# Kernel tuning notes

Hardware: AMD Instinct MI355X
Metric: run time of the kernel (lower is better)

## Reference

```python
import jax, jax.numpy as jnp
import numpy as np

NEG = -1e30  # effective -inf that stays finite in fp32 under cumsum


def _log_semiring_scan(m, v):
    """Solve a[u] = logaddexp(v[u], m[u] + a[u-1]) along the last axis
    via an associative scan in the (logaddexp, +) semiring."""
    def op(a, b):
        am, av = a
        bm, bv = b
        return (am + bm, jnp.logaddexp(bv, bm + av))
    return jax.lax.associative_scan(op, (m, v), axis=-1)[1]


def _rnnt_loss(logits, labels, f_len, y_len):
    B, T, U1, V = logits.shape
    U = U1 - 1
    lp = jax.nn.log_softmax(logits, axis=-1)              # [B,T,U+1,V]
    blank = lp[..., 0]                                    # [B,T,U+1]
    # emit[b,t,u] = lp[b,t,u, labels[b,u]]  (gather=True path of warp_rnnt)
    emit = jnp.take_along_axis(
        lp[:, :, :U, :], labels[:, None, :, None].astype(jnp.int32), axis=-1
    )[..., 0]                                             # [B,T,U]
    # forbid emitting past the true label length
    u_idx = jnp.arange(U)
    emit = jnp.where(u_idx[None, None, :] < y_len[:, None, None], emit, NEG)

    # alpha[0,u] = sum of first u emit log-probs at t=0
    alpha0 = jnp.concatenate(
        [jnp.zeros((B, 1), lp.dtype), jnp.cumsum(emit[:, 0, :], axis=-1)], axis=-1
    )                                                     # [B,U+1]

    def step(alpha_prev, xs):
        blank_tm1, emit_t = xs                            # [B,U+1], [B,U]
        tmp = alpha_prev + blank_tm1                      # come-from-below term
        m = jnp.concatenate([jnp.full((B, 1), NEG, tmp.dtype), emit_t], axis=-1)
        a = _log_semiring_scan(m, tmp)                    # come-from-left recurrence
        return a, a

    xs = (blank[:, :-1, :].transpose(1, 0, 2), emit[:, 1:, :].transpose(1, 0, 2))
    _, rows = jax.lax.scan(step, alpha0, xs)              # [T-1,B,U+1]
    alphas = jnp.concatenate([alpha0[None], rows], axis=0).transpose(1, 0, 2)  # [B,T,U+1]

    t_last = (f_len - 1).astype(jnp.int32)
    alpha_T = jnp.take_along_axis(alphas, t_last[:, None, None], axis=1)[:, 0, :]
    blank_T = jnp.take_along_axis(blank, t_last[:, None, None], axis=1)[:, 0, :]
    ll = jnp.take_along_axis(alpha_T + blank_T, y_len[:, None].astype(jnp.int32), axis=1)[:, 0]
    return -jnp.mean(ll)  # reduction='mean', average_frames=False


def setup_inputs() -> dict:
    key = jax.random.key(0)
    k1, k2, k3, k4 = jax.random.split(key, 4)
    B, T, U, V = 8, 256, 64, 1024
    logits = jax.random.normal(k1, (B, T, U + 1, V), dtype=jnp.float32)
    labels = jax.random.randint(k2, (B, U), 1, V, dtype=jnp.int32)  # blank=0 excluded
    f_len = jax.random.randint(k3, (B,), T // 2, T + 1, dtype=jnp.int32)
    y_len = jax.random.randint(k4, (B,), U // 2, U + 1, dtype=jnp.int32)
    return {"logits": logits, "labels": labels, "f_len": f_len, "y_len": y_len}


def reference(logits, labels, f_len, y_len):
    return _rnnt_loss(logits, labels, f_len, y_len)
```

## Files before the change

### kernel.cpp

```cpp
#include <hip/hip_runtime.h>

#define NEG (-1e30f)

__global__ __launch_bounds__(256) void rnnt_softmax_gather(
    const float* __restrict__ logits, const int* __restrict__ labels,
    const int* __restrict__ f_len, const int* __restrict__ y_len,
    float* __restrict__ blankT, float* __restrict__ emitT,
    int B, int T, int U, int rows)
{
    const int V = 1024;
    int widx = threadIdx.x >> 6;
    int lane = threadIdx.x & 63;
    int r = blockIdx.x * 4 + widx;
    if (r >= rows) return;

    int U1 = U + 1;
    int u  = r % U1;
    int bt = r / U1;
    int b  = bt / T;
    int t  = bt % T;

    if (t >= f_len[b]) return;

    const float*  rowp  = logits + (size_t)r * V;
    const float4* rowp4 = reinterpret_cast<const float4*>(rowp);

    float4 v0 = rowp4[lane];
    float4 v1 = rowp4[lane + 64];
    float4 v2 = rowp4[lane + 128];
    float4 v3 = rowp4[lane + 192];

    bool has_emit = (u < U);
    float lab_logit = 0.f;
    if (has_emit && lane == 0) {
        int label = labels[b * U + u];
        lab_logit = rowp[label];
    }

    float m = fmaxf(fmaxf(fmaxf(v0.x, v0.y), fmaxf(v0.z, v0.w)),
                    fmaxf(fmaxf(v1.x, v1.y), fmaxf(v1.z, v1.w)));
    m = fmaxf(m, fmaxf(fmaxf(v2.x, v2.y), fmaxf(v2.z, v2.w)));
    m = fmaxf(m, fmaxf(fmaxf(v3.x, v3.y), fmaxf(v3.z, v3.w)));
    #pragma unroll
    for (int off = 32; off; off >>= 1) m = fmaxf(m, __shfl_xor(m, off));

    float s = __expf(v0.x - m) + __expf(v0.y - m) + __expf(v0.z - m) + __expf(v0.w - m)
            + __expf(v1.x - m) + __expf(v1.y - m) + __expf(v1.z - m) + __expf(v1.w - m)
            + __expf(v2.x - m) + __expf(v2.y - m) + __expf(v2.z - m) + __expf(v2.w - m)
            + __expf(v3.x - m) + __expf(v3.y - m) + __expf(v3.z - m) + __expf(v3.w - m);
    #pragma unroll
    for (int off = 32; off; off >>= 1) s += __shfl_xor(s, off);

    if (lane == 0) {
        float lse = m + __logf(s);
        blankT[((size_t)b * U1 + u) * T + t] = v0.x - lse;
        if (has_emit) {
            float e = lab_logit - lse;
            if (u >= y_len[b]) e = NEG;
            emitT[((size_t)b * U + u) * T + t] = e;
        }
    }
}

__global__ __launch_bounds__(128) void rnnt_alpha(
    const float* __restrict__ blankT, const float* __restrict__ emitT,
    const int* __restrict__ f_len, const int* __restrict__ y_len,
    float* __restrict__ out, int B, int T, int U)
{
    int b = blockIdx.x;
    int u = threadIdx.x;
    int U1 = U + 1;

    __shared__ float sbuf[2][80];

    int t_last = f_len[b] - 1;
    int yl     = y_len[b];
    const float* blank_row = blankT + ((size_t)b * U1 + u) * T;
    const float* emit_row  = emitT  + ((size_t)b * U  + u) * T;

    float a      = NEG;
    float bl_cur = NEG;
    float em_cur = (u < U) ? emit_row[0] : 0.f;

    int D = t_last + yl;
    for (int d = 0; d <= D; ++d) {
        int t = d - u;
        if (u < U1 && t >= 0 && t < T) {
            float x = (t > 0) ? a + bl_cur : NEG;
            float y = (u > 0) ? sbuf[(d ^ 1) & 1][u - 1] : NEG;
            float mx = fmaxf(x, y);
            float mn = fminf(x, y);
            float na = mx + __logf(1.f + __expf(mn - mx));
            a = (d == 0) ? 0.f : na;
            if (u < U) sbuf[d & 1][u] = a + em_cur;
            if (t == t_last && u == yl) {
                float ll = a + blank_row[t_last];
                atomicAdd(out, -ll * (1.0f / (float)B));
            }
            bl_cur = blank_row[t];
            if (u < U && t + 1 < T) em_cur = emit_row[t + 1];
        }
        __syncthreads();
    }
}

extern "C" void kernel_launch(void* const* d_in, const int* in_sizes, int n_in,
                              void* d_out, int out_size, void* d_ws, size_t ws_size,
                              hipStream_t stream) {
    const float* logits = (const float*)d_in[0];
    const int*   labels = (const int*)d_in[1];
    const int*   f_len  = (const int*)d_in[2];
    const int*   y_len  = (const int*)d_in[3];

    const int V  = 1024;
    int B  = in_sizes[2];
    int U  = in_sizes[1] / B;
    int U1 = U + 1;
    int T  = (int)((long long)in_sizes[0] / ((long long)B * U1 * V));
    int rows = B * T * U1;

    float* blankT = (float*)d_ws;
    float* emitT  = blankT + (size_t)B * U1 * T;

    hipMemsetAsync(d_out, 0, sizeof(float), stream);

    dim3 grid1((rows + 3) / 4);
    rnnt_softmax_gather<<<grid1, 256, 0, stream>>>(
        logits, labels, f_len, y_len, blankT, emitT, B, T, U, rows);

    rnnt_alpha<<<B, 128, 0, stream>>>(
        blankT, emitT, f_len, y_len, (float*)d_out, B, T, U);
}
```

Baseline: 753.6 us.

## Store blank/emit in diagonal layout and run alpha wavefront in a single wave

The softmax kernel now skips rows with u beyond the label length and writes blank and emit log-probs into a diagonal-major layout indexed by (t+u, u). The alpha recurrence runs as one 64-lane wavefront that passes the left neighbour with shuffles instead of shared memory and block barriers. An extra register path handles u=64, and loads are prefetched eight diagonals ahead. This removes the per-diagonal __syncthreads and the strided reads, but adds special-case logic for the 65th column and reads diagonal entries the skipped rows never write.

```diff
diff --git a/kernel.cpp b/kernel.cpp
--- a/kernel.cpp
+++ b/kernel.cpp
@@ -5,7 +5,7 @@
 __global__ __launch_bounds__(256) void rnnt_softmax_gather(
     const float* __restrict__ logits, const int* __restrict__ labels,
     const int* __restrict__ f_len, const int* __restrict__ y_len,
-    float* __restrict__ blankT, float* __restrict__ emitT,
+    float* __restrict__ blankD, float* __restrict__ emitD,
     int B, int T, int U, int rows)
 {
     const int V = 1024;
@@ -20,22 +20,22 @@
     int b  = bt / T;
     int t  = bt % T;
 
-    if (t >= f_len[b]) return;
+    if (t >= f_len[b] || u > y_len[b]) return;
 
     const float*  rowp  = logits + (size_t)r * V;
     const float4* rowp4 = reinterpret_cast<const float4*>(rowp);
+
+    bool has_emit = (u < U) && (u < y_len[b]);
+    float lab_logit = 0.f;
+    if (has_emit && lane == 0) {
+        int label = labels[b * U + u];
+        lab_logit = rowp[label];
+    }
 
     float4 v0 = rowp4[lane];
     float4 v1 = rowp4[lane + 64];
     float4 v2 = rowp4[lane + 128];
     float4 v3 = rowp4[lane + 192];
-
-    bool has_emit = (u < U);
-    float lab_logit = 0.f;
-    if (has_emit && lane == 0) {
-        int label = labels[b * U + u];
-        lab_logit = rowp[label];
-    }
 
     float m = fmaxf(fmaxf(fmaxf(v0.x, v0.y), fmaxf(v0.z, v0.w)),
                     fmaxf(fmaxf(v1.x, v1.y), fmaxf(v1.z, v1.w)));
@@ -53,17 +53,16 @@
 
     if (lane == 0) {
         float lse = m + __logf(s);
-        blankT[((size_t)b * U1 + u) * T + t] = v0.x - lse;
+        int d = t + u;
+        blankD[((size_t)b * (T + U) + d) * U1 + u] = v0.x - lse;
         if (has_emit) {
-            float e = lab_logit - lse;
-            if (u >= y_len[b]) e = NEG;
-            emitT[((size_t)b * U + u) * T + t] = e;
+            emitD[((size_t)b * (T + U) + d) * U + u] = lab_logit - lse;
         }
     }
 }
 
-__global__ __launch_bounds__(128) void rnnt_alpha(
-    const float* __restrict__ blankT, const float* __restrict__ emitT,
+__global__ __launch_bounds__(64) void rnnt_alpha(
+    const float* __restrict__ blankD, const float* __restrict__ emitD,
     const int* __restrict__ f_len, const int* __restrict__ y_len,
     float* __restrict__ out, int B, int T, int U)
 {
@@ -71,36 +70,71 @@
     int u = threadIdx.x;
     int U1 = U + 1;
 
-    __shared__ float sbuf[2][80];
-
     int t_last = f_len[b] - 1;
     int yl     = y_len[b];
-    const float* blank_row = blankT + ((size_t)b * U1 + u) * T;
-    const float* emit_row  = emitT  + ((size_t)b * U  + u) * T;
+    const float* bDb = blankD + (size_t)b * (T + U) * U1;
+    const float* eDb = emitD  + (size_t)b * (T + U) * U;
+    int D = t_last + yl;
+    bool has64 = (yl == U) && (U == 64);
+    float invB = 1.0f / (float)B;
 
-    float a      = NEG;
-    float bl_cur = NEG;
-    float em_cur = (u < U) ? emit_row[0] : 0.f;
+    constexpr int PD = 8;
+    float pb[PD], pe[PD], pb64[PD];
+    #pragma unroll
+    for (int k = 0; k < PD; ++k) {
+        int d  = (k <= D) ? k : D;
+        int ib = (d >= 1) ? d - 1 : 0;
+        pb[k]   = bDb[(size_t)ib * U1 + u];
+        pe[k]   = eDb[(size_t)d  * U  + u];
+        pb64[k] = bDb[(size_t)ib * U1 + 64];
+    }
 
-    int D = t_last + yl;
-    for (int d = 0; d <= D; ++d) {
-        int t = d - u;
-        if (u < U1 && t >= 0 && t < T) {
-            float x = (t > 0) ? a + bl_cur : NEG;
-            float y = (u > 0) ? sbuf[(d ^ 1) & 1][u - 1] : NEG;
-            float mx = fmaxf(x, y);
-            float mn = fminf(x, y);
-            float na = mx + __logf(1.f + __expf(mn - mx));
-            a = (d == 0) ? 0.f : na;
-            if (u < U) sbuf[d & 1][u] = a + em_cur;
-            if (t == t_last && u == yl) {
-                float ll = a + blank_row[t_last];
-                atomicAdd(out, -ll * (1.0f / (float)B));
+    float a = NEG, z = NEG, a64 = NEG;
+
+    for (int dd = 0; dd <= D; dd += PD) {
+        #pragma unroll
+        for (int k = 0; k < PD; ++k) {
+            int d = dd + k;
+            if (d <= D) {
+                float z_old  = z;
+                float z_left = __shfl_up(z, 1);
+                int  t   = d - u;
+                bool act = (t >= 0) && (t <= t_last) && (u <= yl);
+
+                float x = (act && t > 0) ? a + pb[k] : NEG;
+                float y = (act && u > 0) ? z_left   : NEG;
+                float mx = fmaxf(x, y), mn = fminf(x, y);
+                float na = mx + __logf(1.0f + __expf(mn - mx));
+                if (d == 0 && u == 0) na = 0.0f;
+                if (act) a = na;
+                z = act ? (a + ((u < yl) ? pe[k] : NEG)) : NEG;
+
+                if (act && t == t_last && u == yl) {
+                    float bl = bDb[(size_t)(t_last + yl) * U1 + yl];
+                    atomicAdd(out, -(a + bl) * invB);
+                }
+
+                if (has64) {
+                    int  t64    = d - 64;
+                    bool a64act = (u == 63) && (t64 >= 0) && (t64 <= t_last);
+                    float x4 = (a64act && t64 > 0) ? a64 + pb64[k] : NEG;
+                    float y4 = a64act ? z_old : NEG;
+                    float mx4 = fmaxf(x4, y4), mn4 = fminf(x4, y4);
+                    float na4 = mx4 + __logf(1.0f + __expf(mn4 - mx4));
+                    if (a64act) a64 = na4;
+                    if (a64act && t64 == t_last) {
+                        float bl4 = bDb[(size_t)(t_last + 64) * U1 + 64];
+                        atomicAdd(out, -(a64 + bl4) * invB);
+                    }
+                }
+
+                int dn  = d + PD; if (dn > D) dn = D;
+                int ibn = (dn >= 1) ? dn - 1 : 0;
+                pb[k]   = bDb[(size_t)ibn * U1 + u];
+                pe[k]   = eDb[(size_t)dn  * U  + u];
+                pb64[k] = bDb[(size_t)ibn * U1 + 64];
             }
-            bl_cur = blank_row[t];
-            if (u < U && t + 1 < T) em_cur = emit_row[t + 1];
         }
-        __syncthreads();
     }
 }
 
@@ -119,15 +153,15 @@
     int T  = (int)((long long)in_sizes[0] / ((long long)B * U1 * V));
     int rows = B * T * U1;
 
-    float* blankT = (float*)d_ws;
-    float* emitT  = blankT + (size_t)B * U1 * T;
+    float* blankD = (float*)d_ws;
+    float* emitD  = blankD + (size_t)B * (T + U) * U1;
 
     hipMemsetAsync(d_out, 0, sizeof(float), stream);
 
     dim3 grid1((rows + 3) / 4);
     rnnt_softmax_gather<<<grid1, 256, 0, stream>>>(
-        logits, labels, f_len, y_len, blankT, emitT, B, T, U, rows);
+        logits, labels, f_len, y_len, blankD, emitD, B, T, U, rows);
 
-    rnnt_alpha<<<B, 128, 0, stream>>>(
-        blankT, emitT, f_len, y_len, (float*)d_out, B, T, U);
+    rnnt_alpha<<<B, 64, 0, stream>>>(
+        blankD, emitD, f_len, y_len, (float*)d_out, B, T, U);
 }
```

After: 724.4 us. 3.9% less time.
